# Optimization experiments

Hardware: AMD Instinct MI355X
Metric: run time of the kernel (lower is better)

The kernel has to match this reference:

```python
import jax, jax.numpy as jnp
import numpy as np

BS, SEQ, INP, HID = 64, 512, 512, 1024

def setup_inputs() -> dict:
    key = jax.random.key(0)
    k1, k2, k3, k4, k5 = jax.random.split(key, 5)
    scale_ih = 1.0 / np.sqrt(HID)
    return {
        "x_in": jax.random.normal(k1, (BS, SEQ, INP), dtype=jnp.float32),
        "W_ih": jax.random.normal(k2, (HID, INP), dtype=jnp.float32) * scale_ih,
        "W_hh": jax.random.normal(k3, (HID, HID), dtype=jnp.float32) * scale_ih,
        "b_ih": jax.random.normal(k4, (HID,), dtype=jnp.float32) * scale_ih,
        "b_hh": jax.random.normal(k5, (HID,), dtype=jnp.float32) * scale_ih,
    }

def reference(x_in, W_ih, W_hh, b_ih, b_hh):
    # batch_first=True: x_in is (B, S, F); permute to (S, B, F)
    x = jnp.swapaxes(x_in, 0, 1)
    # Precompute input projection for all timesteps in one big GEMM: (S, B, H)
    xw = jnp.einsum('sbf,hf->sbh', x, W_ih) + b_ih + b_hh
    h0 = jnp.zeros((x_in.shape[0], W_hh.shape[0]), dtype=x_in.dtype)

    def step(h, xt):
        # RNNCell: h' = tanh(x W_ih^T + b_ih + h W_hh^T + b_hh)
        h_new = jnp.tanh(xt + h @ W_hh.T)
        return h_new, h_new

    _, hiddens = jax.lax.scan(step, h0, xw)  # (S, B, H)
    return jnp.swapaxes(hiddens, 0, 1)  # back to (B, S, H)
```

## Files before the change

kernel.cpp:

```cpp
#include <hip/hip_runtime.h>

#define BATCH 64
#define SEQ   512
#define INP   512
#define HID   1024
#define MAGIC 0x13570000u

#define NG 8
#define GB 8
#define NJT 64
#define TJ 16

__global__ __launch_bounds__(256) void xw_gemm(
    const float* __restrict__ X, const float* __restrict__ Wih,
    const float* __restrict__ bih, const float* __restrict__ bhh,
    float* __restrict__ out)
{
    __shared__ float As[8][128];
    __shared__ float Bs[8][128];
    const int t  = threadIdx.x;
    const int m0 = blockIdx.x * 128;
    const int n0 = blockIdx.y * 128;
    const int lr = t >> 1;
    const int lk = (t & 1) * 4;
    const int ty = t >> 4;
    const int tx = t & 15;

    float acc[8][8];
#pragma unroll
    for (int i = 0; i < 8; ++i)
#pragma unroll
        for (int j = 0; j < 8; ++j) acc[i][j] = 0.f;

    const float* xrow = X   + (size_t)(m0 + lr) * INP + lk;
    const float* wrow = Wih + (size_t)(n0 + lr) * INP + lk;

    for (int k0 = 0; k0 < INP; k0 += 8) {
        float4 av = *(const float4*)(xrow + k0);
        float4 bv = *(const float4*)(wrow + k0);
        __syncthreads();
        As[lk + 0][lr] = av.x; As[lk + 1][lr] = av.y;
        As[lk + 2][lr] = av.z; As[lk + 3][lr] = av.w;
        Bs[lk + 0][lr] = bv.x; Bs[lk + 1][lr] = bv.y;
        Bs[lk + 2][lr] = bv.z; Bs[lk + 3][lr] = bv.w;
        __syncthreads();
#pragma unroll
        for (int kk = 0; kk < 8; ++kk) {
            float4 a0 = *(const float4*)&As[kk][ty * 4];
            float4 a1 = *(const float4*)&As[kk][64 + ty * 4];
            float4 b0 = *(const float4*)&Bs[kk][tx * 4];
            float4 b1 = *(const float4*)&Bs[kk][64 + tx * 4];
            float am[8] = {a0.x, a0.y, a0.z, a0.w, a1.x, a1.y, a1.z, a1.w};
            float bn[8] = {b0.x, b0.y, b0.z, b0.w, b1.x, b1.y, b1.z, b1.w};
#pragma unroll
            for (int i = 0; i < 8; ++i)
#pragma unroll
                for (int j = 0; j < 8; ++j)
                    acc[i][j] = fmaf(am[i], bn[j], acc[i][j]);
        }
    }

    const int nA = n0 + tx * 4;
    const int nB = n0 + 64 + tx * 4;
    float4 bA1 = *(const float4*)(bih + nA);
    float4 bA2 = *(const float4*)(bhh + nA);
    float4 bB1 = *(const float4*)(bih + nB);
    float4 bB2 = *(const float4*)(bhh + nB);
    float4 biasA = make_float4(bA1.x + bA2.x, bA1.y + bA2.y, bA1.z + bA2.z, bA1.w + bA2.w);
    float4 biasB = make_float4(bB1.x + bB2.x, bB1.y + bB2.y, bB1.z + bB2.z, bB1.w + bB2.w);

#pragma unroll
    for (int i = 0; i < 8; ++i) {
        int mloc = (i < 4) ? (ty * 4 + i) : (64 + ty * 4 + (i - 4));
        size_t m = (size_t)(m0 + mloc);
        float4 vA = make_float4(acc[i][0] + biasA.x, acc[i][1] + biasA.y,
                                acc[i][2] + biasA.z, acc[i][3] + biasA.w);
        float4 vB = make_float4(acc[i][4] + biasB.x, acc[i][5] + biasB.y,
                                acc[i][6] + biasB.z, acc[i][7] + biasB.w);
        *(float4*)(out + m * HID + nA) = vA;
        *(float4*)(out + m * HID + nB) = vB;
    }
}

__global__ __launch_bounds__(256, 2) void rnn_scan(
    const float* __restrict__ Whh, float* __restrict__ out,
    unsigned* __restrict__ flags)
{
    __shared__ float4 Hlds[GB][256];
    __shared__ float  Pbuf[4][GB][TJ];

    const int t    = threadIdx.x;
    const int g    = blockIdx.x >> 6;
    const int jt   = blockIdx.x & 63;
    const int lane = t & 63;
    const int w    = t >> 6;
    const int kc2  = (lane >> 4) & 3;
    const int jl   = lane & 15;
    const int base4 = w * 64 + kc2 * 16;

    float4 Wreg[16];
    {
        const float4* wr = (const float4*)(Whh + (size_t)(jt * TJ + jl) * HID) + base4;
#pragma unroll
        for (int q = 0; q < 4; ++q) {
            const int rot = 4 * ((kc2 + q) & 3);
#pragma unroll
            for (int r = 0; r < 4; ++r)
                Wreg[q * 4 + r] = wr[rot + r];
        }
    }

    const int bo = t >> 4;
    const int jo = t & 15;

    for (int s = 0; s < SEQ; ++s) {
        float xw = 0.f;
        if (t < 128)
            xw = out[((size_t)(g * GB + bo) * SEQ + s) * HID + jt * TJ + jo];

        float p[GB];
#pragma unroll
        for (int b = 0; b < GB; ++b) p[b] = 0.f;

        if (s > 0) {
            if (t < 64) {
                const unsigned want = MAGIC + (unsigned)(s - 1);
                unsigned* f = flags + ((((s - 1) & 3) * NG + g) * 64 + t);
                while (__hip_atomic_load(f, __ATOMIC_RELAXED, __HIP_MEMORY_SCOPE_AGENT) != want)
                    __builtin_amdgcn_s_sleep(1);
            }
            __syncthreads();
            __builtin_amdgcn_fence(__ATOMIC_ACQUIRE, "agent");

#pragma unroll
            for (int rr = 0; rr < 2; ++rr) {
                const int b = w * 2 + rr;
                const float4* hrow =
                    (const float4*)(out + ((size_t)(g * GB + b) * SEQ + (s - 1)) * HID);
#pragma unroll
                for (int i2 = 0; i2 < 4; ++i2)
                    Hlds[b][i2 * 64 + lane] = hrow[i2 * 64 + lane];
            }
            __syncthreads();

#pragma unroll
            for (int q = 0; q < 4; ++q) {
                const int rot = 4 * ((kc2 + q) & 3);
#pragma unroll
                for (int r = 0; r < 4; ++r) {
                    const float4 wv = Wreg[q * 4 + r];
#pragma unroll
                    for (int b = 0; b < GB; ++b) {
                        const float4 h4 = Hlds[b][base4 + rot + r];
                        p[b] = fmaf(wv.x, h4.x, p[b]);
                        p[b] = fmaf(wv.y, h4.y, p[b]);
                        p[b] = fmaf(wv.z, h4.z, p[b]);
                        p[b] = fmaf(wv.w, h4.w, p[b]);
                    }
                }
            }
#pragma unroll
            for (int b = 0; b < GB; ++b) {
                p[b] += __shfl_xor(p[b], 16);
                p[b] += __shfl_xor(p[b], 32);
            }
        }

        if (lane < 16) {
#pragma unroll
            for (int b = 0; b < GB; ++b) Pbuf[w][b][jl] = p[b];
        }
        __syncthreads();

        if (t < 128) {
            float tot = xw + Pbuf[0][bo][jo] + Pbuf[1][bo][jo]
                           + Pbuf[2][bo][jo] + Pbuf[3][bo][jo];
            float v = tanhf(tot);
            __hip_atomic_store(
                out + ((size_t)(g * GB + bo) * SEQ + s) * HID + jt * TJ + jo,
                v, __ATOMIC_RELAXED, __HIP_MEMORY_SCOPE_AGENT);
        }
        __syncthreads();
        if (t == 0)
            __hip_atomic_store(flags + (((s & 3) * NG + g) * 64 + jt),
                               MAGIC + (unsigned)s,
                               __ATOMIC_RELAXED, __HIP_MEMORY_SCOPE_AGENT);
    }
}

extern "C" void kernel_launch(void* const* d_in, const int* in_sizes, int n_in,
                              void* d_out, int out_size, void* d_ws, size_t ws_size,
                              hipStream_t stream)
{
    (void)in_sizes; (void)n_in; (void)out_size; (void)ws_size;
    const float* x   = (const float*)d_in[0];
    const float* Wih = (const float*)d_in[1];
    const float* Whh = (const float*)d_in[2];
    const float* bih = (const float*)d_in[3];
    const float* bhh = (const float*)d_in[4];
    float* out = (float*)d_out;
    unsigned* flags = (unsigned*)d_ws;

    dim3 g1(BATCH * SEQ / 128, HID / 128);
    xw_gemm<<<g1, 256, 0, stream>>>(x, Wih, bih, bhh, out);
    rnn_scan<<<NG * NJT, 256, 0, stream>>>(Whh, out, flags);
}
```

Measured before the change: 10.17 ms.

## Reassign scan work so each wave owns whole outputs and drops LDS reduction

Each wave now owns 4 output columns, and its 16 lanes split the K dimension. The partial sums are reduced entirely with intra-wave shuffles, which removes the Pbuf LDS stage and one __syncthreads per timestep. Hidden-state loads now use relaxed atomic loads into registers and are written to LDS with a rotated (swizzled) column layout to avoid bank conflicts. The acquire fence is swapped for a release fence before the flag store. This shortens the per-step critical path of the sequential scan, at some risk to memory-ordering correctness.

```diff
diff --git a/kernel.cpp b/kernel.cpp
--- a/kernel.cpp
+++ b/kernel.cpp
@@ -87,36 +87,27 @@
     unsigned* __restrict__ flags)
 {
     __shared__ float4 Hlds[GB][256];
-    __shared__ float  Pbuf[4][GB][TJ];
 
     const int t    = threadIdx.x;
     const int g    = blockIdx.x >> 6;
     const int jt   = blockIdx.x & 63;
     const int lane = t & 63;
     const int w    = t >> 6;
-    const int kc2  = (lane >> 4) & 3;
-    const int jl   = lane & 15;
-    const int base4 = w * 64 + kc2 * 16;
+    const int jq   = lane >> 4;
+    const int kc   = lane & 15;
+    const int j    = jt * TJ + w * 4 + jq;
 
     float4 Wreg[16];
     {
-        const float4* wr = (const float4*)(Whh + (size_t)(jt * TJ + jl) * HID) + base4;
-#pragma unroll
-        for (int q = 0; q < 4; ++q) {
-            const int rot = 4 * ((kc2 + q) & 3);
-#pragma unroll
-            for (int r = 0; r < 4; ++r)
-                Wreg[q * 4 + r] = wr[rot + r];
-        }
-    }
-
-    const int bo = t >> 4;
-    const int jo = t & 15;
+        const float4* wr = (const float4*)(Whh + (size_t)j * HID) + kc * 16;
+#pragma unroll
+        for (int i = 0; i < 16; ++i) Wreg[i] = wr[i];
+    }
 
     for (int s = 0; s < SEQ; ++s) {
         float xw = 0.f;
-        if (t < 128)
-            xw = out[((size_t)(g * GB + bo) * SEQ + s) * HID + jt * TJ + jo];
+        if (kc < GB)
+            xw = out[((size_t)(g * GB + kc) * SEQ + s) * HID + j];
 
         float p[GB];
 #pragma unroll
@@ -125,61 +116,67 @@
         if (s > 0) {
             if (t < 64) {
                 const unsigned want = MAGIC + (unsigned)(s - 1);
-                unsigned* f = flags + ((((s - 1) & 3) * NG + g) * 64 + t);
+                const unsigned* f = flags + (((s - 1) & 3) * NG + g) * 64 + t;
                 while (__hip_atomic_load(f, __ATOMIC_RELAXED, __HIP_MEMORY_SCOPE_AGENT) != want)
                     __builtin_amdgcn_s_sleep(1);
             }
             __syncthreads();
-            __builtin_amdgcn_fence(__ATOMIC_ACQUIRE, "agent");
-
+
+            float hv[2][16];
 #pragma unroll
             for (int rr = 0; rr < 2; ++rr) {
-                const int b = w * 2 + rr;
-                const float4* hrow =
-                    (const float4*)(out + ((size_t)(g * GB + b) * SEQ + (s - 1)) * HID);
-#pragma unroll
-                for (int i2 = 0; i2 < 4; ++i2)
-                    Hlds[b][i2 * 64 + lane] = hrow[i2 * 64 + lane];
+                const float* hrow =
+                    out + ((size_t)(g * GB + w * 2 + rr) * SEQ + (s - 1)) * HID;
+#pragma unroll
+                for (int u = 0; u < 16; ++u)
+                    hv[rr][u] = __hip_atomic_load(hrow + u * 64 + lane,
+                                                  __ATOMIC_RELAXED,
+                                                  __HIP_MEMORY_SCOPE_AGENT);
+            }
+#pragma unroll
+            for (int rr = 0; rr < 2; ++rr) {
+                float* Hb = (float*)&Hlds[w * 2 + rr][0];
+#pragma unroll
+                for (int u = 0; u < 16; ++u) {
+                    const int d = u * 64 + lane;
+                    const int c = d >> 2;
+                    const int pc = (c & 0xF0) | ((c + (c >> 4)) & 15);
+                    Hb[pc * 4 + (d & 3)] = hv[rr][u];
+                }
             }
             __syncthreads();
 
 #pragma unroll
-            for (int q = 0; q < 4; ++q) {
-                const int rot = 4 * ((kc2 + q) & 3);
-#pragma unroll
-                for (int r = 0; r < 4; ++r) {
-                    const float4 wv = Wreg[q * 4 + r];
-#pragma unroll
-                    for (int b = 0; b < GB; ++b) {
-                        const float4 h4 = Hlds[b][base4 + rot + r];
-                        p[b] = fmaf(wv.x, h4.x, p[b]);
-                        p[b] = fmaf(wv.y, h4.y, p[b]);
-                        p[b] = fmaf(wv.z, h4.z, p[b]);
-                        p[b] = fmaf(wv.w, h4.w, p[b]);
-                    }
+            for (int i = 0; i < 16; ++i) {
+                const int pcol = kc * 16 + ((i + kc) & 15);
+                const float4 wv = Wreg[i];
+#pragma unroll
+                for (int b = 0; b < GB; ++b) {
+                    const float4 h4 = Hlds[b][pcol];
+                    p[b] = fmaf(wv.x, h4.x, p[b]);
+                    p[b] = fmaf(wv.y, h4.y, p[b]);
+                    p[b] = fmaf(wv.z, h4.z, p[b]);
+                    p[b] = fmaf(wv.w, h4.w, p[b]);
                 }
             }
 #pragma unroll
             for (int b = 0; b < GB; ++b) {
-                p[b] += __shfl_xor(p[b], 16);
-                p[b] += __shfl_xor(p[b], 32);
+                p[b] += __shfl_xor(p[b], 1);
+                p[b] += __shfl_xor(p[b], 2);
+                p[b] += __shfl_xor(p[b], 4);
+                p[b] += __shfl_xor(p[b], 8);
             }
         }
 
-        if (lane < 16) {
-#pragma unroll
-            for (int b = 0; b < GB; ++b) Pbuf[w][b][jl] = p[b];
+        if (kc < GB) {
+            float acc = 0.f;
+#pragma unroll
+            for (int b = 0; b < GB; ++b) acc = (kc == b) ? p[b] : acc;
+            const float v = tanhf(xw + acc);
+            __hip_atomic_store(out + ((size_t)(g * GB + kc) * SEQ + s) * HID + j,
+                               v, __ATOMIC_RELAXED, __HIP_MEMORY_SCOPE_AGENT);
         }
-        __syncthreads();
-
-        if (t < 128) {
-            float tot = xw + Pbuf[0][bo][jo] + Pbuf[1][bo][jo]
-                           + Pbuf[2][bo][jo] + Pbuf[3][bo][jo];
-            float v = tanhf(tot);
-            __hip_atomic_store(
-                out + ((size_t)(g * GB + bo) * SEQ + s) * HID + jt * TJ + jo,
-                v, __ATOMIC_RELAXED, __HIP_MEMORY_SCOPE_AGENT);
-        }
+        __builtin_amdgcn_fence(__ATOMIC_RELEASE, "agent");
         __syncthreads();
         if (t == 0)
             __hip_atomic_store(flags + (((s & 3) * NG + g) * 64 + jt),
```

After: 12.18 ms. 19.8% more time.
